# Optimization experiments

Hardware: AMD Instinct MI355X
Metric: run time of the kernel (lower is better)

The kernel has to match this reference:

```python
import jax, jax.numpy as jnp
import numpy as np

# Config matching init_kwargs
C, H_IMG, W_IMG = 3, 224, 224
N_PATCHES = 14
PS = H_IMG // N_PATCHES            # 16
INPUT_D = C * PS * PS              # 768
HID = 768
N_HEADS = 12
DH = HID // N_HEADS                # 64
N_BLOCKS = 12
MLP_RATIO = 4
SEQ = N_PATCHES * N_PATCHES + 1    # 197
EPS = 1e-5


def _pos_embed():
    # sin on even dims, cos on odd dims, exponent uses (j - j%2)/d  (faithful to loop)
    i = jnp.arange(SEQ, dtype=jnp.float32)[:, None]
    j = jnp.arange(HID, dtype=jnp.float32)[None, :]
    expo = (j - jnp.mod(j, 2.0)) / HID
    ang = i / jnp.power(10000.0, expo)
    return jnp.where(jnp.mod(jnp.arange(HID), 2) == 0, jnp.sin(ang), jnp.cos(ang))


def setup_inputs() -> dict:
    key = jax.random.key(0)
    ks = jax.random.split(key, 16)
    s = 0.02
    d_ff = MLP_RATIO * HID
    inp = {
        'images': jax.random.normal(ks[0], (16, C, H_IMG, W_IMG), dtype=jnp.float32),
        'w_map': jax.random.normal(ks[1], (HID, INPUT_D), dtype=jnp.float32) * s,
        'b_map': jnp.zeros((HID,), dtype=jnp.float32),
        'class_token': jax.random.uniform(ks[2], (1, HID), dtype=jnp.float32),
        'pos_embed': _pos_embed(),
        'qw': jax.random.normal(ks[3], (N_BLOCKS, N_HEADS, DH, DH), dtype=jnp.float32) * s,
        'qb': jnp.zeros((N_BLOCKS, N_HEADS, DH), dtype=jnp.float32),
        'kw': jax.random.normal(ks[4], (N_BLOCKS, N_HEADS, DH, DH), dtype=jnp.float32) * s,
        'kb': jnp.zeros((N_BLOCKS, N_HEADS, DH), dtype=jnp.float32),
        'vw': jax.random.normal(ks[5], (N_BLOCKS, N_HEADS, DH, DH), dtype=jnp.float32) * s,
        'vb': jnp.zeros((N_BLOCKS, N_HEADS, DH), dtype=jnp.float32),
        'ln1_w': jnp.ones((N_BLOCKS, HID), dtype=jnp.float32),
        'ln1_b': jnp.zeros((N_BLOCKS, HID), dtype=jnp.float32),
        'ln2_w': jnp.ones((N_BLOCKS, HID), dtype=jnp.float32),
        'ln2_b': jnp.zeros((N_BLOCKS, HID), dtype=jnp.float32),
        'mlp_w1': jax.random.normal(ks[6], (N_BLOCKS, d_ff, HID), dtype=jnp.float32) * s,
        'mlp_b1': jnp.zeros((N_BLOCKS, d_ff), dtype=jnp.float32),
        'mlp_w2': jax.random.normal(ks[7], (N_BLOCKS, HID, d_ff), dtype=jnp.float32) * s,
        'mlp_b2': jnp.zeros((N_BLOCKS, HID), dtype=jnp.float32),
    }
    return inp


def _layernorm(x, w, b):
    mu = jnp.mean(x, axis=-1, keepdims=True)
    var = jnp.mean(jnp.square(x - mu), axis=-1, keepdims=True)
    return (x - mu) * jax.lax.rsqrt(var + EPS) * w + b


def _patchify(images):
    # [N,C,H,W] -> [N, np^2, C*ps*ps]; per-patch flatten order is (c, ph, pw)
    n = images.shape[0]
    x = images.reshape(n, C, N_PATCHES, PS, N_PATCHES, PS)
    x = x.transpose(0, 2, 4, 1, 3, 5)  # n, pi, pj, c, ph, pw
    return x.reshape(n, N_PATCHES * N_PATCHES, INPUT_D)


def _msa(x, qw, qb, kw, kb, vw, vb):
    # x: [B,S,D]; per-head Linear on head slices; torch Linear: y = x @ W.T + b
    b_, s_, _ = x.shape
    xh = x.reshape(b_, s_, N_HEADS, DH)
    q = jnp.einsum('bshd,hod->bsho', xh, qw) + qb
    k = jnp.einsum('bshd,hod->bsho', xh, kw) + kb
    v = jnp.einsum('bshd,hod->bsho', xh, vw) + vb
    attn = jax.nn.softmax(jnp.einsum('bsho,btho->bhst', q, k) / (DH ** 0.5), axis=-1)
    out = jnp.einsum('bhst,btho->bsho', attn, v)
    return out.reshape(b_, s_, HID)


def reference(images, w_map, b_map, class_token, pos_embed, qw, qb, kw, kb, vw, vb,
              ln1_w, ln1_b, ln2_w, ln2_b, mlp_w1, mlp_b1, mlp_w2, mlp_b2):
    patches = _patchify(images)                       # [N, 196, 768]
    tokens = patches @ w_map.T + b_map                # [N, 196, HID]
    n = tokens.shape[0]
    cls = jnp.broadcast_to(class_token[None], (n, 1, HID))
    out = jnp.concatenate([cls, tokens], axis=1) + pos_embed[None]  # [N, SEQ, HID]
    for l in range(N_BLOCKS):
        out = out + _msa(_layernorm(out, ln1_w[l], ln1_b[l]),
                         qw[l], qb[l], kw[l], kb[l], vw[l], vb[l])
        h = _layernorm(out, ln2_w[l], ln2_b[l])
        h = jax.nn.gelu(h @ mlp_w1[l].T + mlp_b1[l], approximate=False)
        out = out + (h @ mlp_w2[l].T + mlp_b2[l])
    return out
```

## Files before the change

kernel.cpp:

```cpp
#include <hip/hip_runtime.h>
#include <hip/hip_bf16.h>
#include <math.h>

typedef __attribute__((ext_vector_type(4))) float f32x4;
typedef __attribute__((ext_vector_type(8))) __bf16 bf16x8;
typedef __attribute__((ext_vector_type(8))) short short8;
typedef __attribute__((ext_vector_type(4))) unsigned short us4;
typedef __attribute__((ext_vector_type(8))) unsigned short us8;

#define B_    16
#define SEQ_  197
#define TOK_  3152
#define HID_  768
#define MPAD_ 3200
#define NP_   3136
#define SP_   224
#define DFF_  3072
#define PSZ_  (MPAD_ * HID_)

__device__ __forceinline__ unsigned short f2bf(float x) {
  union { float f; unsigned int u; } v; v.f = x;
  unsigned int r = v.u + 0x7fffu + ((v.u >> 16) & 1u);
  return (unsigned short)(r >> 16);
}

__device__ __forceinline__ float bf2f(unsigned short u) {
  union { unsigned int i; float f; } v; v.i = ((unsigned int)u) << 16; return v.f;
}

__device__ __forceinline__ f32x4 mfma16(bf16x8 a, bf16x8 b, f32x4 c) {
  return __builtin_amdgcn_mfma_f32_16x16x32_bf16(a, b, c, 0, 0, 0);
}

__device__ __forceinline__ void cp16(const void* g, void* l) {
  __builtin_amdgcn_global_load_lds((__attribute__((address_space(1))) void*)(g),
                                   (__attribute__((address_space(3))) void*)(l),
                                   16, 0, 0);
}

__device__ __forceinline__ float gelu_f(float x) {
  float y = x * (1.5957691216f + 0.0713548162f * x * x);
  float e = __expf(y);
  float r = 1.0f / (1.0f + e);
  return x - x * r;
}

__device__ __forceinline__ void conv8(const float* __restrict__ s, unsigned short* __restrict__ d, int c) {
  const float* sp = s + (size_t)c * 8;
  f32x4 v0 = *(const f32x4*)sp;
  f32x4 v1 = *(const f32x4*)(sp + 4);
  us8 o;
  o[0] = f2bf(v0[0]); o[1] = f2bf(v0[1]); o[2] = f2bf(v0[2]); o[3] = f2bf(v0[3]);
  o[4] = f2bf(v1[0]); o[5] = f2bf(v1[1]); o[6] = f2bf(v1[2]); o[7] = f2bf(v1[3]);
  *(us8*)(d + (size_t)c * 8) = o;
}

__global__ __launch_bounds__(256) void patchcls_kernel(const float* __restrict__ img,
                                                       unsigned short* __restrict__ Pb,
                                                       const float* __restrict__ ct,
                                                       const float* __restrict__ pos,
                                                       float* __restrict__ X,
                                                       const float* __restrict__ wmap,
                                                       unsigned short* __restrict__ Wmb,
                                                       const float* __restrict__ cw1,
                                                       unsigned short* __restrict__ cd1,
                                                       const float* __restrict__ cw2,
                                                       unsigned short* __restrict__ cd2) {
  int bid = blockIdx.x;
  if (bid >= 2736) {
    int bb = bid - 2736;
    const float* s; unsigned short* d;
    if (bb < 1152) { s = cw1; d = cd1; } else { s = cw2; d = cd2; bb -= 1152; }
    conv8(s, d, bb * 256 + threadIdx.x);
    return;
  }
  if (bid >= 2448) {
    int c = (bid - 2448) * 256 + threadIdx.x;
    conv8(wmap, Wmb, c);
    return;
  }
  if (bid >= 2400) {
    int j = (bid - 2400) * 256 + threadIdx.x;
    if (j < B_ * HID_) {
      int b = j / HID_, t = j - b * HID_;
      X[(size_t)b * SEQ_ * HID_ + t] = ct[t] + pos[t];
    }
    return;
  }
  int gid = bid * 256 + threadIdx.x;
  int m = gid / 192;
  int j4 = (gid - m * 192) * 4;
  us4 o;
  if (m < NP_) {
    int n = m / 196, p = m - n * 196;
    int pi = p / 14, pj = p - pi * 14;
    int c = j4 >> 8, rem = j4 & 255, ph = rem >> 4, pw = rem & 15;
    const float* src = img + (((size_t)(n * 3 + c) * 224 + pi * 16 + ph) * 224 + pj * 16 + pw);
    f32x4 v = *(const f32x4*)src;
    o[0] = f2bf(v[0]); o[1] = f2bf(v[1]); o[2] = f2bf(v[2]); o[3] = f2bf(v[3]);
  } else {
    o[0] = 0; o[1] = 0; o[2] = 0; o[3] = 0;
  }
  *(us4*)(Pb + (size_t)m * HID_ + j4) = o;
}

__global__ __launch_bounds__(256) void convw_kernel(const float* __restrict__ s1, unsigned short* __restrict__ d1,
                                                    const float* __restrict__ s2, unsigned short* __restrict__ d2,
                                                    int nchunks) {
  int half = gridDim.x >> 1;
  int b = blockIdx.x;
  const float* s; unsigned short* d;
  if (b < half) { s = s1; d = d1; } else { s = s2; d = d2; b -= half; }
  int c = b * 256 + threadIdx.x;
  if (c >= nchunks) return;
  conv8(s, d, c);
}

__global__ __launch_bounds__(256) void gemm_embed(const unsigned short* __restrict__ A,
                                                  const unsigned short* __restrict__ Bw,
                                                  const float* __restrict__ bias,
                                                  const float* __restrict__ pos,
                                                  float* __restrict__ Xout) {
  constexpr int MI = 2, NJ = 2, BM = 64, BN = 64;
  __shared__ unsigned short As[BM * 64];
  __shared__ unsigned short Bs[BN * 64];
  const int tid = threadIdx.x;
  const int w = tid >> 6, lane = tid & 63;
  const int lr = lane & 15, kg = lane >> 4;
  int bid = blockIdx.x;
  int cpx = gridDim.x >> 3;
  int swz = (bid & 7) * cpx + (bid >> 3);
  const int by = swz / 12, bx = swz - by * 12;
  const int m0 = by * BM, n0 = bx * BN;
  const int wr = w >> 1, wc = w & 1;
  const f32x4 z4 = {0.f, 0.f, 0.f, 0.f};
  f32x4 acc[MI][NJ];
#pragma unroll
  for (int i = 0; i < MI; ++i)
#pragma unroll
    for (int j = 0; j < NJ; ++j) acc[i][j] = z4;
  for (int k0 = 0; k0 < 768; k0 += 64) {
#pragma unroll
    for (int is = 0; is < MI; ++is) {
      int chunk = is * 256 + tid;
      int row = chunk >> 3, cc = (chunk & 7) * 8;
      cp16(A + (size_t)(m0 + row) * 768 + k0 + cc, As + is * 2048 + w * 512);
    }
#pragma unroll
    for (int is = 0; is < NJ; ++is) {
      int chunk = is * 256 + tid;
      int row = chunk >> 3, cc = (chunk & 7) * 8;
      cp16(Bw + (size_t)(n0 + row) * 768 + k0 + cc, Bs + is * 2048 + w * 512);
    }
    __syncthreads();
#pragma unroll
    for (int kk = 0; kk < 64; kk += 32) {
      bf16x8 af[MI], bfr[NJ];
#pragma unroll
      for (int i = 0; i < MI; ++i)
        af[i] = *(const bf16x8*)&As[(wr * (BM / 2) + i * 16 + lr) * 64 + kk + kg * 8];
#pragma unroll
      for (int j = 0; j < NJ; ++j)
        bfr[j] = *(const bf16x8*)&Bs[(wc * (BN / 2) + j * 16 + lr) * 64 + kk + kg * 8];
#pragma unroll
      for (int i = 0; i < MI; ++i)
#pragma unroll
        for (int j = 0; j < NJ; ++j)
          acc[i][j] = mfma16(af[i], bfr[j], acc[i][j]);
    }
    __syncthreads();
  }
#pragma unroll
  for (int i = 0; i < MI; ++i) {
    int mbase = m0 + wr * (BM / 2) + i * 16 + kg * 4;
#pragma unroll
    for (int j = 0; j < NJ; ++j) {
      int col = n0 + wc * (BN / 2) + j * 16 + lr;
#pragma unroll
      for (int qr = 0; qr < 4; ++qr) {
        int m = mbase + qr;
        if (m < NP_) {
          int nimg = m / 196;
          int tok = m + nimg + 1;
          int prow = m - nimg * 196 + 1;
          Xout[(size_t)tok * HID_ + col] = acc[i][j][qr] + bias[col] + pos[(size_t)prow * HID_ + col];
        }
      }
    }
  }
}

template<int EPI, int NT>
__global__ __launch_bounds__(512, 2) void gemm4b(const unsigned short* __restrict__ A,
                                                 const unsigned short* __restrict__ Bw,
                                                 int ldk, int gx, int gy,
                                                 const float* __restrict__ bias,
                                                 unsigned short* __restrict__ Pout,
                                                 unsigned short* __restrict__ Hout) {
  __shared__ unsigned short lds4[32768];
  const int tid = threadIdx.x;
  const int wid = tid >> 6, lane = tid & 63;
  const int lr = lane & 15, kg = lane >> 4;
  const int wm = wid >> 2, wn = wid & 3;
  const int nwg = gridDim.x;
  const int q = nwg >> 3, r = nwg & 7;
  const int xcd = blockIdx.x & 7, idx = blockIdx.x >> 3;
  const int wgid = (xcd < r ? xcd * (q + 1) : r * (q + 1) + (xcd - r) * q) + idx;
  const int bx = wgid % gx;
  const int rest = wgid / gx;
  const int by = rest % gy;
  const int z = rest / gy;
  const int m0 = by * 128, n0 = bx * 128;
  const unsigned short* Abase = A + (size_t)m0 * ldk + z * (NT * 32);
  const unsigned short* Bbase = Bw + (size_t)n0 * ldk + z * (NT * 32);

  const int ra = tid >> 2, ka = (tid & 3) * 8;
  const int wbase = wid * 512;

#pragma unroll
  for (int t = 0; t < 3; ++t) {
    unsigned short* lb = lds4 + t * 8192;
    cp16(Abase + (size_t)ra * ldk + ka + t * 32, lb + wbase);
    cp16(Bbase + (size_t)ra * ldk + ka + t * 32, lb + 4096 + wbase);
  }

  const f32x4 z4 = {0.f, 0.f, 0.f, 0.f};
  f32x4 acc[4][2];
#pragma unroll
  for (int i = 0; i < 4; ++i)
#pragma unroll
    for (int j = 0; j < 2; ++j) acc[i][j] = z4;

#pragma unroll 1
  for (int k = 0; k < NT; ++k) {
    asm volatile("s_waitcnt vmcnt(4)" ::: "memory");
    __builtin_amdgcn_s_barrier();
    __builtin_amdgcn_sched_barrier(0);
    const unsigned short* lp = lds4 + (k & 3) * 8192;
    const int tn = k + 3;
    const int ts = (tn >= NT) ? tn - NT : tn;
    unsigned short* tb = lds4 + (tn & 3) * 8192;
    bf16x8 af[4], bfr[2];
#pragma unroll
    for (int i = 0; i < 4; ++i)
      af[i] = *(const bf16x8*)(lp + (wm * 64 + i * 16 + lr) * 32 + kg * 8);
#pragma unroll
    for (int j = 0; j < 2; ++j)
      bfr[j] = *(const bf16x8*)(lp + 4096 + (wn * 32 + j * 16 + lr) * 32 + kg * 8);
    cp16(Abase + (size_t)ra * ldk + ka + ts * 32, tb + wbase);
    cp16(Bbase + (size_t)ra * ldk + ka + ts * 32, tb + 4096 + wbase);
    __builtin_amdgcn_s_barrier();
    __builtin_amdgcn_s_setprio(1);
#pragma unroll
    for (int i = 0; i < 4; ++i)
#pragma unroll
      for (int j = 0; j < 2; ++j) acc[i][j] = mfma16(af[i], bfr[j], acc[i][j]);
    __builtin_amdgcn_s_setprio(0);
  }

#pragma unroll
  for (int i = 0; i < 4; ++i) {
    int mbase = m0 + wm * 64 + i * 16 + kg * 4;
#pragma unroll
    for (int j = 0; j < 2; ++j) {
      int col = n0 + wn * 32 + j * 16 + lr;
      float bv = (EPI == 1) ? bias[col] : 0.f;
#pragma unroll
      for (int qr = 0; qr < 4; ++qr) {
        int m = mbase + qr;
        if (m < TOK_) {
          float v = acc[i][j][qr];
          if (EPI == 1) {
            Hout[(size_t)m * 3072 + col] = f2bf(gelu_f(v + bv));
          } else {
            Pout[(size_t)z * PSZ_ + (size_t)m * 768 + col] = f2bf(v);
          }
        }
      }
    }
  }
}

template<int MODE>
__global__ __launch_bounds__(256) void ln_kernel(float* __restrict__ X,
                                                 const unsigned short* __restrict__ P, const float* __restrict__ pb,
                                                 const float* __restrict__ gw, const float* __restrict__ gb,
                                                 unsigned short* __restrict__ Y,
                                                 const float* __restrict__ cw1, unsigned short* __restrict__ cd1,
                                                 const float* __restrict__ cw2, unsigned short* __restrict__ cd2) {
  int bb = (int)blockIdx.x - 800;
  if (bb >= 0) {
    const float* s; unsigned short* d;
    if (bb < 1152) { s = cw1; d = cd1; } else { s = cw2; d = cd2; bb -= 1152; }
    conv8(s, d, bb * 256 + threadIdx.x);
    return;
  }
  int row = blockIdx.x * 4 + (threadIdx.x >> 6);
  int lane = threadIdx.x & 63;
  if (row >= MPAD_) return;
  size_t base = (size_t)row * HID_;
  if (row >= TOK_) {
    us4 zz; zz[0] = 0; zz[1] = 0; zz[2] = 0; zz[3] = 0;
#pragma unroll
    for (int i = 0; i < 3; ++i) *(us4*)(Y + base + i * 256 + lane * 4) = zz;
    return;
  }
  f32x4 xv[3];
  float s1 = 0.f, s2 = 0.f;
#pragma unroll
  for (int i = 0; i < 3; ++i) {
    int cb = i * 256 + lane * 4;
    f32x4 v = *(const f32x4*)(X + base + cb);
    if (MODE == 2) {
      const unsigned short* pp = P + base + cb;
      us4 p0 = *(const us4*)(pp);
      us4 p1 = *(const us4*)(pp + PSZ_);
      f32x4 bb2 = *(const f32x4*)(pb + cb);
#pragma unroll
      for (int e = 0; e < 4; ++e)
        v[e] += bf2f(p0[e]) + bf2f(p1[e]) + bb2[e];
      *(f32x4*)(X + base + cb) = v;
    }
    xv[i] = v;
    s1 += v[0] + v[1] + v[2] + v[3];
    s2 += v[0] * v[0] + v[1] * v[1] + v[2] * v[2] + v[3] * v[3];
  }
#pragma unroll
  for (int d = 1; d < 64; d <<= 1) {
    s1 += __shfl_xor(s1, d);
    s2 += __shfl_xor(s2, d);
  }
  float mu = s1 * (1.f / 768.f);
  float var = s2 * (1.f / 768.f) - mu * mu;
  float rs = rsqrtf(var + 1e-5f);
#pragma unroll
  for (int i = 0; i < 3; ++i) {
    int cb = i * 256 + lane * 4;
    us4 o;
#pragma unroll
    for (int e = 0; e < 4; ++e)
      o[e] = f2bf((xv[i][e] - mu) * rs * gw[cb + e] + gb[cb + e]);
    *(us4*)(Y + base + cb) = o;
  }
}

__global__ __launch_bounds__(256) void redfin_kernel(float* __restrict__ X, const unsigned short* __restrict__ P,
                                                     const float* __restrict__ b2) {
  int i = blockIdx.x * 256 + threadIdx.x;
  if (i >= TOK_ * 192) return;
  int m = i / 192, c4 = (i - m * 192) * 4;
  size_t off = (size_t)m * HID_ + c4;
  f32x4 v = *(const f32x4*)(X + off);
  const unsigned short* pp = P + off;
  us4 p0 = *(const us4*)(pp);
  us4 p1 = *(const us4*)(pp + PSZ_);
  f32x4 bb = *(const f32x4*)(b2 + c4);
#pragma unroll
  for (int e = 0; e < 4; ++e)
    v[e] += bf2f(p0[e]) + bf2f(p1[e]) + bb[e];
  *(f32x4*)(X + off) = v;
}

__device__ __forceinline__ void loadw_frags(const float* __restrict__ W, int lr, int kg, bf16x8* wf) {
#pragma unroll
  for (int j = 0; j < 4; ++j)
#pragma unroll
    for (int kk = 0; kk < 2; ++kk) {
      const float* wp = W + (j * 16 + lr) * 64 + kk * 32 + kg * 8;
      f32x4 w0 = *(const f32x4*)wp;
      f32x4 w1 = *(const f32x4*)(wp + 4);
      short8 t;
      t[0] = (short)f2bf(w0[0]); t[1] = (short)f2bf(w0[1]); t[2] = (short)f2bf(w0[2]); t[3] = (short)f2bf(w0[3]);
      t[4] = (short)f2bf(w1[0]); t[5] = (short)f2bf(w1[1]); t[6] = (short)f2bf(w1[2]); t[7] = (short)f2bf(w1[3]);
      wf[j * 2 + kk] = __builtin_bit_cast(bf16x8, t);
    }
}

__global__ __launch_bounds__(256) void qkvattn_kernel(const unsigned short* __restrict__ Y,
                                                      const float* __restrict__ qw, const float* __restrict__ qb,
                                                      const float* __restrict__ kw, const float* __restrict__ kb,
                                                      const float* __restrict__ vw, const float* __restrict__ vb,
                                                      float* __restrict__ X) {
  __shared__ unsigned short klds[SP_ * 64];
  __shared__ unsigned short vtlds[64 * 232];
  __shared__ unsigned short plds[4 * 16 * 232];
  const int bh = blockIdx.x;
  const int b = bh / 12, h = bh % 12;
  const int wv = threadIdx.x >> 6, lane = threadIdx.x & 63;
  const int lr = lane & 15, kg = lane >> 4;
  const int ntile = (wv < 2) ? 4 : 3;
  const f32x4 z4 = {0.f, 0.f, 0.f, 0.f};
  const short8 zs = {0, 0, 0, 0, 0, 0, 0, 0};

  {
    bf16x8 wf[8];
    loadw_frags(qw + h * 4096, lr, kg, wf);
    float qbias[4];
#pragma unroll
    for (int j = 0; j < 4; ++j) qbias[j] = qb[h * 64 + j * 16 + lr];
#pragma unroll
    for (int i = 0; i < 4; ++i) {
      if (i < ntile) {
        int t = wv + 4 * i;
        int s = t * 16 + lr;
        bf16x8 a0 = __builtin_bit_cast(bf16x8, zs), a1 = a0;
        if (s < SEQ_) {
          const unsigned short* yp = Y + (size_t)(b * SEQ_ + s) * HID_ + h * 64 + kg * 8;
          a0 = *(const bf16x8*)yp;
          a1 = *(const bf16x8*)(yp + 32);
        }
        f32x4 acc[4] = {z4, z4, z4, z4};
#pragma unroll
        for (int j = 0; j < 4; ++j) {
          acc[j] = mfma16(a0, wf[j * 2 + 0], acc[j]);
          acc[j] = mfma16(a1, wf[j * 2 + 1], acc[j]);
        }
#pragma unroll
        for (int j = 0; j < 4; ++j)
#pragma unroll
          for (int qr = 0; qr < 4; ++qr) {
            int row = t * 16 + kg * 4 + qr;
            int col = (j * 16 + lr) ^ ((row & 7) << 3);
            klds[row * 64 + col] = f2bf((acc[j][qr] + qbias[j]) * 0.125f);
          }
      }
    }
  }
  __syncthreads();
  bf16x8 aq[4][2];
#pragma unroll
  for (int i = 0; i < 4; ++i) {
    if (i < ntile) {
      int row = (wv + 4 * i) * 16 + lr;
      int sw = (row & 7) << 3;
      aq[i][0] = *(const bf16x8*)&klds[row * 64 + ((kg * 8) ^ sw)];
      aq[i][1] = *(const bf16x8*)&klds[row * 64 + ((32 + kg * 8) ^ sw)];
    }
  }
  __syncthreads();
  {
    bf16x8 wkf[8], wvf[8];
    loadw_frags(kw + h * 4096, lr, kg, wkf);
    loadw_frags(vw + h * 4096, lr, kg, wvf);
    float kbias[4], vbias[4];
#pragma unroll
    for (int j = 0; j < 4; ++j) {
      kbias[j] = kb[h * 64 + j * 16 + lr];
      vbias[j] = vb[h * 64 + j * 16 + lr];
    }
#pragma unroll
    for (int i = 0; i < 4; ++i) {
      if (i < ntile) {
        int t = wv + 4 * i;
        int s = t * 16 + lr;
        bf16x8 a0 = __builtin_bit_cast(bf16x8, zs), a1 = a0;
        if (s < SEQ_) {
          const unsigned short* yp = Y + (size_t)(b * SEQ_ + s) * HID_ + h * 64 + kg * 8;
          a0 = *(const bf16x8*)yp;
          a1 = *(const bf16x8*)(yp + 32);
        }
        f32x4 ak[4] = {z4, z4, z4, z4};
        f32x4 av[4] = {z4, z4, z4, z4};
#pragma unroll
        for (int j = 0; j < 4; ++j) {
          ak[j] = mfma16(a0, wkf[j * 2 + 0], ak[j]);
          ak[j] = mfma16(a1, wkf[j * 2 + 1], ak[j]);
          av[j] = mfma16(a0, wvf[j * 2 + 0], av[j]);
          av[j] = mfma16(a1, wvf[j * 2 + 1], av[j]);
        }
#pragma unroll
        for (int j = 0; j < 4; ++j) {
#pragma unroll
          for (int qr = 0; qr < 4; ++qr) {
            int row = t * 16 + kg * 4 + qr;
            int col = (j * 16 + lr) ^ ((row & 7) << 3);
            klds[row * 64 + col] = f2bf(ak[j][qr] + kbias[j]);
          }
          us4 pk;
          pk[0] = f2bf(av[j][0] + vbias[j]); pk[1] = f2bf(av[j][1] + vbias[j]);
          pk[2] = f2bf(av[j][2] + vbias[j]); pk[3] = f2bf(av[j][3] + vbias[j]);
          *(us4*)&vtlds[(j * 16 + lr) * 232 + t * 16 + kg * 4] = pk;
        }
      }
    }
  }
  __syncthreads();
  unsigned short* P = plds + wv * 16 * 232;
  {
    int rr = lane >> 2, c0 = 208 + (lane & 3) * 4;
    us4 zz; zz[0] = 0; zz[1] = 0; zz[2] = 0; zz[3] = 0;
    *(us4*)&P[rr * 232 + c0] = zz;
  }
#pragma unroll
  for (int i = 0; i < 4; ++i) {
    if (i < ntile) {
      int t = wv + 4 * i;
      f32x4 s[13];
#pragma unroll
      for (int nt = 0; nt < 13; ++nt) {
        int row = nt * 16 + lr;
        int sw = (row & 7) << 3;
        bf16x8 b0 = *(const bf16x8*)&klds[row * 64 + ((kg * 8) ^ sw)];
        bf16x8 b1 = *(const bf16x8*)&klds[row * 64 + ((32 + kg * 8) ^ sw)];
        f32x4 acc = mfma16(aq[i][0], b0, z4);
        s[nt] = mfma16(aq[i][1], b1, acc);
      }
#pragma unroll
      for (int qr = 0; qr < 4; ++qr) {
        float mx = -1e30f;
#pragma unroll
        for (int nt = 0; nt < 13; ++nt) {
          float v = (nt == 12 && lr >= 5) ? -1e30f : s[nt][qr];
          mx = fmaxf(mx, v);
        }
        mx = fmaxf(mx, __shfl_xor(mx, 1));
        mx = fmaxf(mx, __shfl_xor(mx, 2));
        mx = fmaxf(mx, __shfl_xor(mx, 4));
        mx = fmaxf(mx, __shfl_xor(mx, 8));
        float sum = 0.f;
#pragma unroll
        for (int nt = 0; nt < 13; ++nt) {
          float e = (nt == 12 && lr >= 5) ? 0.f : __expf(s[nt][qr] - mx);
          s[nt][qr] = e;
          sum += e;
        }
        sum += __shfl_xor(sum, 1);
        sum += __shfl_xor(sum, 2);
        sum += __shfl_xor(sum, 4);
        sum += __shfl_xor(sum, 8);
        float inv = 1.f / sum;
#pragma unroll
        for (int nt = 0; nt < 13; ++nt)
          P[(kg * 4 + qr) * 232 + nt * 16 + lr] = f2bf(s[nt][qr] * inv);
      }
      asm volatile("s_waitcnt lgkmcnt(0)" ::: "memory");
      __builtin_amdgcn_sched_barrier(0);
      f32x4 ao[4] = {z4, z4, z4, z4};
#pragma unroll
      for (int kt = 0; kt < 7; ++kt) {
        bf16x8 pa = *(const bf16x8*)&P[lr * 232 + kt * 32 + kg * 8];
#pragma unroll
        for (int j = 0; j < 4; ++j) {
          bf16x8 bv = *(const bf16x8*)&vtlds[(j * 16 + lr) * 232 + kt * 32 + kg * 8];
          ao[j] = mfma16(pa, bv, ao[j]);
        }
      }
#pragma unroll
      for (int j = 0; j < 4; ++j)
#pragma unroll
        for (int qr = 0; qr < 4; ++qr) {
          int ss = t * 16 + kg * 4 + qr;
          if (ss < SEQ_) {
            size_t xi = (size_t)(b * SEQ_ + ss) * HID_ + h * 64 + j * 16 + lr;
            X[xi] += ao[j][qr];
          }
        }
    }
  }
}

extern "C" void kernel_launch(void* const* d_in, const int* in_sizes, int n_in,
                              void* d_out, int out_size, void* d_ws, size_t ws_size,
                              hipStream_t stream) {
  const float* images = (const float*)d_in[0];
  const float* w_map  = (const float*)d_in[1];
  const float* b_map  = (const float*)d_in[2];
  const float* ctok   = (const float*)d_in[3];
  const float* pos    = (const float*)d_in[4];
  const float* qw   = (const float*)d_in[5];
  const float* qb   = (const float*)d_in[6];
  const float* kw   = (const float*)d_in[7];
  const float* kb   = (const float*)d_in[8];
  const float* vw   = (const float*)d_in[9];
  const float* vb   = (const float*)d_in[10];
  const float* ln1w = (const float*)d_in[11];
  const float* ln1b = (const float*)d_in[12];
  const float* ln2w = (const float*)d_in[13];
  const float* ln2b = (const float*)d_in[14];
  const float* w1   = (const float*)d_in[15];
  const float* b1   = (const float*)d_in[16];
  const float* w2   = (const float*)d_in[17];
  const float* b2   = (const float*)d_in[18];

  float* X = (float*)d_out;

  unsigned short* Y    = (unsigned short*)d_ws;
  unsigned short* Wmb  = Y + (size_t)MPAD_ * HID_;
  unsigned short* Hb   = Wmb + (size_t)768 * 768;
  unsigned short* Pp   = Hb + (size_t)MPAD_ * DFF_;
  unsigned short* Wr   = Pp + 2 * (size_t)PSZ_;

  const size_t L1 = (size_t)DFF_ * HID_;
  const size_t need = ((size_t)MPAD_ * HID_ + (size_t)768 * 768 + (size_t)MPAD_ * DFF_ +
                       2 * (size_t)PSZ_ + 24 * L1) * 2;
  const bool big = ws_size >= need;
  unsigned short* W1r = Wr;
  unsigned short* W2r = Wr + (big ? 12 * L1 : L1);

  patchcls_kernel<<<big ? 5040 : 2736, 256, 0, stream>>>(images, Y, ctok, pos, X,
                                                         w_map, Wmb, w1, W1r, w2, W2r);
  gemm_embed<<<600, 256, 0, stream>>>(Y, Wmb, b_map, pos, X);

  for (int l = 0; l < 12; ++l) {
    unsigned short* W1p = big ? W1r + l * L1 : W1r;
    unsigned short* W2p = big ? W2r + l * L1 : W2r;
    if (l == 0)
      ln_kernel<0><<<800, 256, 0, stream>>>(X, nullptr, nullptr,
                                            ln1w + l * 768, ln1b + l * 768, Y,
                                            nullptr, nullptr, nullptr, nullptr);
    else
      ln_kernel<2><<<800, 256, 0, stream>>>(X, Pp, b2 + (l - 1) * 768,
                                            ln1w + l * 768, ln1b + l * 768, Y,
                                            nullptr, nullptr, nullptr, nullptr);
    qkvattn_kernel<<<192, 256, 0, stream>>>(Y,
                                            qw + (size_t)l * 49152, qb + l * 768,
                                            kw + (size_t)l * 49152, kb + l * 768,
                                            vw + (size_t)l * 49152, vb + l * 768,
                                            X);
    const bool cvt = big && (l < 11);
    ln_kernel<0><<<cvt ? 3104 : 800, 256, 0, stream>>>(X, nullptr, nullptr,
                                                       ln2w + l * 768, ln2b + l * 768, Y,
                                                       cvt ? w1 + (size_t)(l + 1) * L1 : nullptr,
                                                       cvt ? W1r + (size_t)(l + 1) * L1 : nullptr,
                                                       cvt ? w2 + (size_t)(l + 1) * L1 : nullptr,
                                                       cvt ? W2r + (size_t)(l + 1) * L1 : nullptr);
    if (!big)
      convw_kernel<<<2304, 256, 0, stream>>>(w1 + (size_t)l * L1, W1p,
                                             w2 + (size_t)l * L1, W2p, 294912);
    gemm4b<1, 24><<<600, 512, 0, stream>>>(Y, W1p, 768, 24, 25, b1 + l * 3072, nullptr, Hb);
    gemm4b<3, 48><<<300, 512, 0, stream>>>(Hb, W2p, 3072, 6, 25, nullptr, Pp, nullptr);
  }
  redfin_kernel<<<2364, 256, 0, stream>>>(X, Pp, b2 + 11 * 768);
}
```

Measured before the change: 1.487 ms.

## Split fused QKV-attention kernel into projection and per-query-tile attention kernels

Replaces the single per-(batch,head) fused QKV+attention kernel, launched as 192 blocks, with two kernels. The first computes the Q, K and transposed V projections across 1152 small blocks and writes them to global scratch, reusing the MLP hidden buffer. The second runs attention with one wave per 16-row query tile across 2496 blocks, reading K and V straight from global memory. This is meant to fill the GPU better than 192 blocks can. The cost is an extra launch, a round trip through global memory for Q, K and V, and K and V being re-read by each query tile instead of staged in LDS.

Result: faster. 1.433 ms (-3.6%).

```diff
diff --git a/kernel.cpp b/kernel.cpp
--- a/kernel.cpp
+++ b/kernel.cpp
@@ -14,9 +14,10 @@
 #define HID_  768
 #define MPAD_ 3200
 #define NP_   3136
-#define SP_   224
 #define DFF_  3072
 #define PSZ_  (MPAD_ * HID_)
+#define QKVP_ 14336
+#define BHN_  192
 
 __device__ __forceinline__ unsigned short f2bf(float x) {
   union { float f; unsigned int u; } v; v.f = x;
@@ -376,187 +377,155 @@
     }
 }
 
-__global__ __launch_bounds__(256) void qkvattn_kernel(const unsigned short* __restrict__ Y,
+__global__ __launch_bounds__(128) void qkvproj_kernel(const unsigned short* __restrict__ Y,
                                                       const float* __restrict__ qw, const float* __restrict__ qb,
                                                       const float* __restrict__ kw, const float* __restrict__ kb,
                                                       const float* __restrict__ vw, const float* __restrict__ vb,
-                                                      float* __restrict__ X) {
-  __shared__ unsigned short klds[SP_ * 64];
-  __shared__ unsigned short vtlds[64 * 232];
-  __shared__ unsigned short plds[4 * 16 * 232];
-  const int bh = blockIdx.x;
-  const int b = bh / 12, h = bh % 12;
+                                                      unsigned short* __restrict__ Qo,
+                                                      unsigned short* __restrict__ Ko,
+                                                      unsigned short* __restrict__ Vto) {
+  const int blk = blockIdx.x;
+  const int half = blk & 1;
+  const int bp = blk >> 1;
+  const int p = bp % 3, bh = bp / 3;
+  const int b = bh / 12, h = bh - b * 12;
   const int wv = threadIdx.x >> 6, lane = threadIdx.x & 63;
   const int lr = lane & 15, kg = lane >> 4;
-  const int ntile = (wv < 2) ? 4 : 3;
+  const int ws = half * 2 + wv;
+  const float* W; const float* bs; unsigned short* out;
+  if (p == 0)      { W = qw + h * 4096; bs = qb + h * 64; out = Qo; }
+  else if (p == 1) { W = kw + h * 4096; bs = kb + h * 64; out = Ko; }
+  else             { W = vw + h * 4096; bs = vb + h * 64; out = Vto; }
+  const float scale = (p == 0) ? 0.125f : 1.0f;
+  bf16x8 wf[8];
+  loadw_frags(W, lr, kg, wf);
+  float bj[4];
+#pragma unroll
+  for (int j = 0; j < 4; ++j) bj[j] = bs[j * 16 + lr];
+  out += (size_t)bh * QKVP_;
   const f32x4 z4 = {0.f, 0.f, 0.f, 0.f};
   const short8 zs = {0, 0, 0, 0, 0, 0, 0, 0};
-
-  {
-    bf16x8 wf[8];
-    loadw_frags(qw + h * 4096, lr, kg, wf);
-    float qbias[4];
-#pragma unroll
-    for (int j = 0; j < 4; ++j) qbias[j] = qb[h * 64 + j * 16 + lr];
-#pragma unroll
-    for (int i = 0; i < 4; ++i) {
-      if (i < ntile) {
-        int t = wv + 4 * i;
-        int s = t * 16 + lr;
-        bf16x8 a0 = __builtin_bit_cast(bf16x8, zs), a1 = a0;
-        if (s < SEQ_) {
-          const unsigned short* yp = Y + (size_t)(b * SEQ_ + s) * HID_ + h * 64 + kg * 8;
-          a0 = *(const bf16x8*)yp;
-          a1 = *(const bf16x8*)(yp + 32);
+#pragma unroll
+  for (int i = 0; i < 4; ++i) {
+    int t = ws + 4 * i;
+    if (t < 14) {
+      int s = t * 16 + lr;
+      bf16x8 a0 = __builtin_bit_cast(bf16x8, zs), a1 = a0;
+      if (s < SEQ_) {
+        const unsigned short* yp = Y + (size_t)(b * SEQ_ + s) * HID_ + h * 64 + kg * 8;
+        a0 = *(const bf16x8*)yp;
+        a1 = *(const bf16x8*)(yp + 32);
+      }
+      f32x4 acc[4] = {z4, z4, z4, z4};
+#pragma unroll
+      for (int j = 0; j < 4; ++j) {
+        acc[j] = mfma16(a0, wf[j * 2 + 0], acc[j]);
+        acc[j] = mfma16(a1, wf[j * 2 + 1], acc[j]);
+      }
+      if (p == 2) {
+#pragma unroll
+        for (int j = 0; j < 4; ++j) {
+          us4 pk;
+#pragma unroll
+          for (int qr = 0; qr < 4; ++qr) {
+            int srow = t * 16 + kg * 4 + qr;
+            pk[qr] = (srow < SEQ_) ? f2bf(acc[j][qr] + bj[j]) : (unsigned short)0;
+          }
+          *(us4*)&out[(j * 16 + lr) * 224 + t * 16 + kg * 4] = pk;
         }
-        f32x4 acc[4] = {z4, z4, z4, z4};
-#pragma unroll
-        for (int j = 0; j < 4; ++j) {
-          acc[j] = mfma16(a0, wf[j * 2 + 0], acc[j]);
-          acc[j] = mfma16(a1, wf[j * 2 + 1], acc[j]);
-        }
+      } else {
 #pragma unroll
         for (int j = 0; j < 4; ++j)
 #pragma unroll
           for (int qr = 0; qr < 4; ++qr) {
             int row = t * 16 + kg * 4 + qr;
-            int col = (j * 16 + lr) ^ ((row & 7) << 3);
-            klds[row * 64 + col] = f2bf((acc[j][qr] + qbias[j]) * 0.125f);
+            out[row * 64 + j * 16 + lr] = f2bf((acc[j][qr] + bj[j]) * scale);
           }
       }
     }
   }
-  __syncthreads();
-  bf16x8 aq[4][2];
-#pragma unroll
-  for (int i = 0; i < 4; ++i) {
-    if (i < ntile) {
-      int row = (wv + 4 * i) * 16 + lr;
-      int sw = (row & 7) << 3;
-      aq[i][0] = *(const bf16x8*)&klds[row * 64 + ((kg * 8) ^ sw)];
-      aq[i][1] = *(const bf16x8*)&klds[row * 64 + ((32 + kg * 8) ^ sw)];
-    }
-  }
-  __syncthreads();
-  {
-    bf16x8 wkf[8], wvf[8];
-    loadw_frags(kw + h * 4096, lr, kg, wkf);
-    loadw_frags(vw + h * 4096, lr, kg, wvf);
-    float kbias[4], vbias[4];
-#pragma unroll
-    for (int j = 0; j < 4; ++j) {
-      kbias[j] = kb[h * 64 + j * 16 + lr];
-      vbias[j] = vb[h * 64 + j * 16 + lr];
-    }
-#pragma unroll
-    for (int i = 0; i < 4; ++i) {
-      if (i < ntile) {
-        int t = wv + 4 * i;
-        int s = t * 16 + lr;
-        bf16x8 a0 = __builtin_bit_cast(bf16x8, zs), a1 = a0;
-        if (s < SEQ_) {
-          const unsigned short* yp = Y + (size_t)(b * SEQ_ + s) * HID_ + h * 64 + kg * 8;
-          a0 = *(const bf16x8*)yp;
-          a1 = *(const bf16x8*)(yp + 32);
-        }
-        f32x4 ak[4] = {z4, z4, z4, z4};
-        f32x4 av[4] = {z4, z4, z4, z4};
-#pragma unroll
-        for (int j = 0; j < 4; ++j) {
-          ak[j] = mfma16(a0, wkf[j * 2 + 0], ak[j]);
-          ak[j] = mfma16(a1, wkf[j * 2 + 1], ak[j]);
-          av[j] = mfma16(a0, wvf[j * 2 + 0], av[j]);
-          av[j] = mfma16(a1, wvf[j * 2 + 1], av[j]);
-        }
-#pragma unroll
-        for (int j = 0; j < 4; ++j) {
-#pragma unroll
-          for (int qr = 0; qr < 4; ++qr) {
-            int row = t * 16 + kg * 4 + qr;
-            int col = (j * 16 + lr) ^ ((row & 7) << 3);
-            klds[row * 64 + col] = f2bf(ak[j][qr] + kbias[j]);
-          }
-          us4 pk;
-          pk[0] = f2bf(av[j][0] + vbias[j]); pk[1] = f2bf(av[j][1] + vbias[j]);
-          pk[2] = f2bf(av[j][2] + vbias[j]); pk[3] = f2bf(av[j][3] + vbias[j]);
-          *(us4*)&vtlds[(j * 16 + lr) * 232 + t * 16 + kg * 4] = pk;
-        }
-      }
-    }
-  }
-  __syncthreads();
-  unsigned short* P = plds + wv * 16 * 232;
+}
+
+__global__ __launch_bounds__(64) void attn_kernel(const unsigned short* __restrict__ Qb,
+                                                  const unsigned short* __restrict__ Kb,
+                                                  const unsigned short* __restrict__ Vtb,
+                                                  float* __restrict__ X) {
+  __shared__ unsigned short plds[16 * 232];
+  const int blk = blockIdx.x;
+  const int qt = blk % 13, bh = blk / 13;
+  const int b = bh / 12, h = bh - b * 12;
+  const int lane = threadIdx.x;
+  const int lr = lane & 15, kg = lane >> 4;
+  const f32x4 z4 = {0.f, 0.f, 0.f, 0.f};
+  const unsigned short* Qp = Qb + (size_t)bh * QKVP_;
+  const unsigned short* Kp = Kb + (size_t)bh * QKVP_;
+  const unsigned short* Vp = Vtb + (size_t)bh * QKVP_;
   {
     int rr = lane >> 2, c0 = 208 + (lane & 3) * 4;
     us4 zz; zz[0] = 0; zz[1] = 0; zz[2] = 0; zz[3] = 0;
-    *(us4*)&P[rr * 232 + c0] = zz;
-  }
-#pragma unroll
-  for (int i = 0; i < 4; ++i) {
-    if (i < ntile) {
-      int t = wv + 4 * i;
-      f32x4 s[13];
-#pragma unroll
-      for (int nt = 0; nt < 13; ++nt) {
-        int row = nt * 16 + lr;
-        int sw = (row & 7) << 3;
-        bf16x8 b0 = *(const bf16x8*)&klds[row * 64 + ((kg * 8) ^ sw)];
-        bf16x8 b1 = *(const bf16x8*)&klds[row * 64 + ((32 + kg * 8) ^ sw)];
-        f32x4 acc = mfma16(aq[i][0], b0, z4);
-        s[nt] = mfma16(aq[i][1], b1, acc);
+    *(us4*)&plds[rr * 232 + c0] = zz;
+  }
+  bf16x8 aq0 = *(const bf16x8*)&Qp[(qt * 16 + lr) * 64 + kg * 8];
+  bf16x8 aq1 = *(const bf16x8*)&Qp[(qt * 16 + lr) * 64 + 32 + kg * 8];
+  f32x4 s[13];
+#pragma unroll
+  for (int nt = 0; nt < 13; ++nt) {
+    const unsigned short* kp = Kp + (nt * 16 + lr) * 64 + kg * 8;
+    bf16x8 b0 = *(const bf16x8*)kp;
+    bf16x8 b1 = *(const bf16x8*)(kp + 32);
+    f32x4 acc = mfma16(aq0, b0, z4);
+    s[nt] = mfma16(aq1, b1, acc);
+  }
+#pragma unroll
+  for (int qr = 0; qr < 4; ++qr) {
+    float mx = -1e30f;
+#pragma unroll
+    for (int nt = 0; nt < 13; ++nt) {
+      float v = (nt == 12 && lr >= 5) ? -1e30f : s[nt][qr];
+      mx = fmaxf(mx, v);
+    }
+    mx = fmaxf(mx, __shfl_xor(mx, 1));
+    mx = fmaxf(mx, __shfl_xor(mx, 2));
+    mx = fmaxf(mx, __shfl_xor(mx, 4));
+    mx = fmaxf(mx, __shfl_xor(mx, 8));
+    float sum = 0.f;
+#pragma unroll
+    for (int nt = 0; nt < 13; ++nt) {
+      float e = (nt == 12 && lr >= 5) ? 0.f : __expf(s[nt][qr] - mx);
+      s[nt][qr] = e;
+      sum += e;
+    }
+    sum += __shfl_xor(sum, 1);
+    sum += __shfl_xor(sum, 2);
+    sum += __shfl_xor(sum, 4);
+    sum += __shfl_xor(sum, 8);
+    float inv = 1.f / sum;
+#pragma unroll
+    for (int nt = 0; nt < 13; ++nt)
+      plds[(kg * 4 + qr) * 232 + nt * 16 + lr] = f2bf(s[nt][qr] * inv);
+  }
+  asm volatile("s_waitcnt lgkmcnt(0)" ::: "memory");
+  __builtin_amdgcn_sched_barrier(0);
+  f32x4 ao[4] = {z4, z4, z4, z4};
+#pragma unroll
+  for (int kt = 0; kt < 7; ++kt) {
+    bf16x8 pa = *(const bf16x8*)&plds[lr * 232 + kt * 32 + kg * 8];
+#pragma unroll
+    for (int j = 0; j < 4; ++j) {
+      bf16x8 bv = *(const bf16x8*)&Vp[(j * 16 + lr) * 224 + kt * 32 + kg * 8];
+      ao[j] = mfma16(pa, bv, ao[j]);
+    }
+  }
+#pragma unroll
+  for (int j = 0; j < 4; ++j)
+#pragma unroll
+    for (int qr = 0; qr < 4; ++qr) {
+      int ss = qt * 16 + kg * 4 + qr;
+      if (ss < SEQ_) {
+        size_t xi = (size_t)(b * SEQ_ + ss) * HID_ + h * 64 + j * 16 + lr;
+        X[xi] += ao[j][qr];
       }
-#pragma unroll
-      for (int qr = 0; qr < 4; ++qr) {
-        float mx = -1e30f;
-#pragma unroll
-        for (int nt = 0; nt < 13; ++nt) {
-          float v = (nt == 12 && lr >= 5) ? -1e30f : s[nt][qr];
-          mx = fmaxf(mx, v);
-        }
-        mx = fmaxf(mx, __shfl_xor(mx, 1));
-        mx = fmaxf(mx, __shfl_xor(mx, 2));
-        mx = fmaxf(mx, __shfl_xor(mx, 4));
-        mx = fmaxf(mx, __shfl_xor(mx, 8));
-        float sum = 0.f;
-#pragma unroll
-        for (int nt = 0; nt < 13; ++nt) {
-          float e = (nt == 12 && lr >= 5) ? 0.f : __expf(s[nt][qr] - mx);
-          s[nt][qr] = e;
-          sum += e;
-        }
-        sum += __shfl_xor(sum, 1);
-        sum += __shfl_xor(sum, 2);
-        sum += __shfl_xor(sum, 4);
-        sum += __shfl_xor(sum, 8);
-        float inv = 1.f / sum;
-#pragma unroll
-        for (int nt = 0; nt < 13; ++nt)
-          P[(kg * 4 + qr) * 232 + nt * 16 + lr] = f2bf(s[nt][qr] * inv);
-      }
-      asm volatile("s_waitcnt lgkmcnt(0)" ::: "memory");
-      __builtin_amdgcn_sched_barrier(0);
-      f32x4 ao[4] = {z4, z4, z4, z4};
-#pragma unroll
-      for (int kt = 0; kt < 7; ++kt) {
-        bf16x8 pa = *(const bf16x8*)&P[lr * 232 + kt * 32 + kg * 8];
-#pragma unroll
-        for (int j = 0; j < 4; ++j) {
-          bf16x8 bv = *(const bf16x8*)&vtlds[(j * 16 + lr) * 232 + kt * 32 + kg * 8];
-          ao[j] = mfma16(pa, bv, ao[j]);
-        }
-      }
-#pragma unroll
-      for (int j = 0; j < 4; ++j)
-#pragma unroll
-        for (int qr = 0; qr < 4; ++qr) {
-          int ss = t * 16 + kg * 4 + qr;
-          if (ss < SEQ_) {
-            size_t xi = (size_t)(b * SEQ_ + ss) * HID_ + h * 64 + j * 16 + lr;
-            X[xi] += ao[j][qr];
-          }
-        }
-    }
-  }
+    }
 }
 
 extern "C" void kernel_launch(void* const* d_in, const int* in_sizes, int n_in,
@@ -590,6 +559,10 @@
   unsigned short* Pp   = Hb + (size_t)MPAD_ * DFF_;
   unsigned short* Wr   = Pp + 2 * (size_t)PSZ_;
 
+  unsigned short* Qb  = Hb;
+  unsigned short* Kb2 = Hb + (size_t)BHN_ * QKVP_;
+  unsigned short* Vtb = Hb + 2 * (size_t)BHN_ * QKVP_;
+
   const size_t L1 = (size_t)DFF_ * HID_;
   const size_t need = ((size_t)MPAD_ * HID_ + (size_t)768 * 768 + (size_t)MPAD_ * DFF_ +
                        2 * (size_t)PSZ_ + 24 * L1) * 2;
@@ -612,11 +585,12 @@
       ln_kernel<2><<<800, 256, 0, stream>>>(X, Pp, b2 + (l - 1) * 768,
                                             ln1w + l * 768, ln1b + l * 768, Y,
                                             nullptr, nullptr, nullptr, nullptr);
-    qkvattn_kernel<<<192, 256, 0, stream>>>(Y,
-                                            qw + (size_t)l * 49152, qb + l * 768,
-                                            kw + (size_t)l * 49152, kb + l * 768,
-                                            vw + (size_t)l * 49152, vb + l * 768,
-                                            X);
+    qkvproj_kernel<<<1152, 128, 0, stream>>>(Y,
+                                             qw + (size_t)l * 49152, qb + l * 768,
+                                             kw + (size_t)l * 49152, kb + l * 768,
+                                             vw + (size_t)l * 49152, vb + l * 768,
+                                             Qb, Kb2, Vtb);
+    attn_kernel<<<2496, 64, 0, stream>>>(Qb, Kb2, Vtb, X);
     const bool cvt = big && (l < 11);
     ln_kernel<0><<<cvt ? 3104 : 800, 256, 0, stream>>>(X, nullptr, nullptr,
                                                        ln2w + l * 768, ln2b + l * 768, Y,
```
